# Optimization experiments

Hardware: AMD Instinct MI355X
Metric: run time of the kernel (lower is better)

The kernel has to match this reference:

```python
import jax, jax.numpy as jnp
import numpy as np

N_NODES = 100000


def gcn_conv(x, src, dst, W, b, n_nodes):
    # PyG GCNConv: h = X W; out[i] = sum_j norm_ij * h[j] + b, with self-loops
    # and symmetric normalization norm_ij = deg(i)^-1/2 * deg(j)^-1/2.
    h = x @ W  # [N, out]
    deg = jax.ops.segment_sum(jnp.ones_like(dst, dtype=h.dtype), dst, num_segments=n_nodes)
    dinv = jnp.where(deg > 0, jax.lax.rsqrt(deg), 0.0)
    norm = dinv[src] * dinv[dst]  # [E]
    msg = h[src] * norm[:, None]  # [E, out] gather + scale
    out = jax.ops.segment_sum(msg, dst, num_segments=n_nodes)  # scatter-add
    return out + b


def setup_inputs() -> dict:
    key = jax.random.key(0)
    k_x, k_e, k_w1, k_w2 = jax.random.split(key, 4)
    in_c, hid, out_c = 128, 64, 32
    x = jax.random.normal(k_x, (N_NODES, in_c), dtype=jnp.float32)
    edge_index = jax.random.randint(k_e, (2, 1600000), 0, N_NODES, dtype=jnp.int32)
    W1 = jax.random.normal(k_w1, (in_c, hid), dtype=jnp.float32) / np.sqrt(in_c)
    b1 = jnp.zeros((hid,), dtype=jnp.float32)
    W2 = jax.random.normal(k_w2, (hid, out_c), dtype=jnp.float32) / np.sqrt(hid)
    b2 = jnp.zeros((out_c,), dtype=jnp.float32)
    return {"x": x, "edge_index": edge_index, "W1": W1, "b1": b1, "W2": W2, "b2": b2}


def reference(x, edge_index, W1, b1, W2, b2):
    n = x.shape[0]
    # add self-loops (GCNConv default)
    loops = jnp.arange(n, dtype=edge_index.dtype)
    src = jnp.concatenate([edge_index[0], loops])
    dst = jnp.concatenate([edge_index[1], loops])
    # faithful to original forward: x = (x*x)/x
    x = (x * x) / x
    h = jax.nn.relu(gcn_conv(x, src, dst, W1, b1, n))
    return gcn_conv(h, src, dst, W2, b2, n)
```

## Files before the change

kernel.cpp:

```cpp
#include <hip/hip_runtime.h>
#include <hip/hip_fp16.h>


#define IN_C 128
#define HID 64
#define OUTC 32
#define BSH 9
#define BSZ 512
#define NSLOT 256
#define EPB 8192
#define BSTRIDE 9216

typedef _Float16 half8 __attribute__((ext_vector_type(8)));
typedef float f32x4 __attribute__((ext_vector_type(4)));

static __host__ __device__ __forceinline__ size_t szt(int a) { return (size_t)a; }

__global__ __launch_bounds__(256) void k_part(const int* __restrict__ src,
                                              const int* __restrict__ dst, int E,
                                              int* __restrict__ bedges,
                                              int* __restrict__ cnt,
                                              int* __restrict__ pre) {
  __shared__ int dbuf[EPB];
  __shared__ int sorted[EPB];
  __shared__ int h[NSLOT];
  __shared__ int off[NSLOT];
  const int tid = threadIdx.x;
  h[tid] = 0;
  __syncthreads();
  const int e0 = blockIdx.x * EPB;
  const int n = min(EPB, E - e0);
  const int nv = n & ~3;
  for (int i = tid * 4; i < nv; i += 1024) {
    int4 d4 = *reinterpret_cast<const int4*>(&dst[e0 + i]);
    dbuf[i + 0] = d4.x; dbuf[i + 1] = d4.y;
    dbuf[i + 2] = d4.z; dbuf[i + 3] = d4.w;
    atomicAdd(&h[d4.x >> BSH], 1);
    atomicAdd(&h[d4.y >> BSH], 1);
    atomicAdd(&h[d4.z >> BSH], 1);
    atomicAdd(&h[d4.w >> BSH], 1);
  }
  for (int i = nv + tid; i < n; i += 256) {
    int d = dst[e0 + i];
    dbuf[i] = d;
    atomicAdd(&h[d >> BSH], 1);
  }
  __syncthreads();
  int v = h[tid];
  off[tid] = v;
  __syncthreads();
  for (int o = 1; o < 256; o <<= 1) {
    int w = (tid >= o) ? off[tid - o] : 0;
    __syncthreads();
    off[tid] += w;
    __syncthreads();
  }
  int excl = off[tid] - v;
  cnt[blockIdx.x * NSLOT + tid] = v;
  pre[blockIdx.x * NSLOT + tid] = excl;
  __syncthreads();
  off[tid] = excl;
  __syncthreads();
  for (int i = tid * 4; i < nv; i += 1024) {
    int4 s4 = *reinterpret_cast<const int4*>(&src[e0 + i]);
    int d0 = dbuf[i], d1 = dbuf[i + 1], d2 = dbuf[i + 2], d3 = dbuf[i + 3];
    int p0 = atomicAdd(&off[d0 >> BSH], 1);
    sorted[p0] = (s4.x << BSH) | (d0 & (BSZ - 1));
    int p1 = atomicAdd(&off[d1 >> BSH], 1);
    sorted[p1] = (s4.y << BSH) | (d1 & (BSZ - 1));
    int p2 = atomicAdd(&off[d2 >> BSH], 1);
    sorted[p2] = (s4.z << BSH) | (d2 & (BSZ - 1));
    int p3 = atomicAdd(&off[d3 >> BSH], 1);
    sorted[p3] = (s4.w << BSH) | (d3 & (BSZ - 1));
  }
  for (int i = nv + tid; i < n; i += 256) {
    int s = src[e0 + i], d = dbuf[i];
    int p = atomicAdd(&off[d >> BSH], 1);
    sorted[p] = (s << BSH) | (d & (BSZ - 1));
  }
  __syncthreads();
  for (int i = tid * 4; i < nv; i += 1024) {
    *reinterpret_cast<int4*>(&bedges[e0 + i]) =
        make_int4(sorted[i], sorted[i + 1], sorted[i + 2], sorted[i + 3]);
  }
  for (int i = nv + tid; i < n; i += 256) bedges[e0 + i] = sorted[i];
}

__global__ __launch_bounds__(256) void k_bucket(const int* __restrict__ bedges,
                                                const int* __restrict__ cnt,
                                                const int* __restrict__ pre,
                                                int B, int E,
                                                int2* __restrict__ rd,
                                                float* __restrict__ dinv,
                                                int* __restrict__ csr, int N) {
  __shared__ int ebuf[BSTRIDE];
  __shared__ int obuf[BSTRIDE];
  __shared__ int h[BSZ];
  __shared__ int pfx[BSZ];
  __shared__ int c2[BSZ];
  __shared__ int sc[256];
  __shared__ int dsto[256];
  const int k = blockIdx.x;
  const int tid = threadIdx.x;
  h[tid] = 0; h[tid + 256] = 0;
  c2[tid] = 0; c2[tid + 256] = 0;
  int c = 0, so = 0;
  if (tid < B) {
    c = cnt[tid * NSLOT + k];
    so = pre[tid * NSLOT + k];
  }
  sc[tid] = c;
  __syncthreads();
  for (int o = 1; o < 256; o <<= 1) {
    int w = (tid >= o) ? sc[tid - o] : 0;
    __syncthreads();
    sc[tid] += w;
    __syncthreads();
  }
  dsto[tid] = sc[tid] - c;
  __syncthreads();
  int total = sc[255];
  int nE = min(total, BSTRIDE);
  if (tid < B && c > 0) {
    int gbase = tid * EPB + so;
    int dbase = dsto[tid];
    for (int j = 0; j < c; ++j) {
      int p = dbase + j;
      if (p < BSTRIDE) ebuf[p] = bedges[gbase + j];
    }
  }
  __syncthreads();
  for (int i = tid; i < nE; i += 256) atomicAdd(&h[ebuf[i] & (BSZ - 1)], 1);
  __syncthreads();
  int a0 = h[2 * tid], a1 = h[2 * tid + 1];
  int s = a0 + a1;
  sc[tid] = s;
  __syncthreads();
  for (int o = 1; o < 256; o <<= 1) {
    int w = (tid >= o) ? sc[tid - o] : 0;
    __syncthreads();
    sc[tid] += w;
    __syncthreads();
  }
  int ex = sc[tid] - s;
  pfx[2 * tid] = ex;
  pfx[2 * tid + 1] = ex + a0;
  __syncthreads();
  const int base = k * BSTRIDE;
  for (int i = tid; i < BSZ; i += 256) {
    int node = k * BSZ + i;
    if (node < N) {
      int dg = h[i];
      rd[node] = make_int2(base + pfx[i], dg);
      dinv[node] = rsqrtf((float)(dg + 1));
    }
  }
  for (int i = tid; i < nE; i += 256) {
    int e = ebuf[i];
    int l = e & (BSZ - 1);
    int p = pfx[l] + atomicAdd(&c2[l], 1);
    obuf[p] = e >> BSH;
  }
  __syncthreads();
  int nv = nE & ~3;
  for (int i = tid * 4; i < nv; i += 1024) {
    *reinterpret_cast<int4*>(&csr[base + i]) =
        make_int4(obuf[i], obuf[i + 1], obuf[i + 2], obuf[i + 3]);
  }
  for (int i = nv + tid; i < nE; i += 256) csr[base + i] = obuf[i];
}

__global__ __launch_bounds__(256) void k_gemm1(
    const float* __restrict__ x, const float* __restrict__ W1,
    const float* __restrict__ dinv, __half* __restrict__ h1s, int N) {
  __shared__ _Float16 bf[4 * 4 * 64 * 8];
  const int tid = threadIdx.x;
  for (int idx = tid; idx < 128 * 64; idx += 256) {
    int k = idx >> 6, c = idx & 63;
    int kc = k >> 5, kk = k & 31;
    int chunk = kk >> 3, j = kk & 7;
    int ct = c >> 4, cl = c & 15;
    bf[(((kc * 4 + ct) * 64) + chunk * 16 + cl) * 8 + j] = (_Float16)W1[idx];
  }
  __syncthreads();

  const int lane = tid & 63, wave = tid >> 6;
  const int row0 = blockIdx.x * 64 + wave * 16;
  const int r_a = lane & 15;
  const int chk = lane >> 4;
  const int arow = min(row0 + r_a, N - 1);
  const float* xp = x + szt(arow) * IN_C + chk * 8;

  f32x4 acc[4];
  #pragma unroll
  for (int ct = 0; ct < 4; ++ct) acc[ct] = (f32x4){0.f, 0.f, 0.f, 0.f};

  #pragma unroll
  for (int kc = 0; kc < 4; ++kc) {
    float4 a0 = *reinterpret_cast<const float4*>(xp + kc * 32);
    float4 a1v = *reinterpret_cast<const float4*>(xp + kc * 32 + 4);
    half8 af;
    af[0] = (_Float16)a0.x;  af[1] = (_Float16)a0.y;
    af[2] = (_Float16)a0.z;  af[3] = (_Float16)a0.w;
    af[4] = (_Float16)a1v.x; af[5] = (_Float16)a1v.y;
    af[6] = (_Float16)a1v.z; af[7] = (_Float16)a1v.w;
    #pragma unroll
    for (int ct = 0; ct < 4; ++ct) {
      half8 bfrag = *reinterpret_cast<const half8*>(&bf[(((kc * 4 + ct) * 64) + lane) * 8]);
      acc[ct] = __builtin_amdgcn_mfma_f32_16x16x32_f16(af, bfrag, acc[ct], 0, 0, 0);
    }
  }
  #pragma unroll
  for (int r = 0; r < 4; ++r) {
    int drow = row0 + chk * 4 + r;
    if (drow < N) {
      float di = dinv[drow];
      #pragma unroll
      for (int ct = 0; ct < 4; ++ct)
        h1s[szt(drow) * HID + ct * 16 + r_a] = (__half)(acc[ct][r] * di);
    }
  }
}

__global__ __launch_bounds__(256) void k_agg1(
    const __half* __restrict__ h1s, const int* __restrict__ csr,
    const int2* __restrict__ rd, const float* __restrict__ dinv,
    const float* __restrict__ b1, __half* __restrict__ a1, int N) {
  const int tid = threadIdx.x;
  int node = blockIdx.x * 32 + (tid >> 3);
  if (node >= N) return;
  const int l = tid & 7;
  const int g0 = (tid & 63) & ~7;
  const _Float16* hp = (const _Float16*)h1s;

  half8 selfv = *reinterpret_cast<const half8*>(hp + szt(node) * HID + l * 8);
  float acc[8];
  #pragma unroll
  for (int q = 0; q < 8; ++q) acc[q] = (float)selfv[q];

  int2 v = rd[node];
  int base = v.x, cnt = v.y;
  if (cnt > 0) {
    int last = base + cnt - 1;
    int myidx = csr[min(base + l, last)];
    for (int j = 0; j < cnt; j += 8) {
      int id[8];
      #pragma unroll
      for (int u = 0; u < 8; ++u) id[u] = __shfl(myidx, g0 + u);
      half8 gv[8];
      #pragma unroll
      for (int u = 0; u < 8; ++u)
        gv[u] = *reinterpret_cast<const half8*>(hp + szt(id[u]) * HID + l * 8);
      int jn = j + 8;
      if (jn < cnt) myidx = csr[min(base + jn + l, last)];
      #pragma unroll
      for (int u = 0; u < 8; ++u) {
        bool ok = (j + u) < cnt;
        #pragma unroll
        for (int q = 0; q < 8; ++q) acc[q] += ok ? (float)gv[u][q] : 0.0f;
      }
    }
  }
  float di = dinv[node];
  float4 bb0 = *reinterpret_cast<const float4*>(b1 + l * 8);
  float4 bb1 = *reinterpret_cast<const float4*>(b1 + l * 8 + 4);
  half8 o;
  o[0] = (_Float16)fmaxf(di * acc[0] + bb0.x, 0.f);
  o[1] = (_Float16)fmaxf(di * acc[1] + bb0.y, 0.f);
  o[2] = (_Float16)fmaxf(di * acc[2] + bb0.z, 0.f);
  o[3] = (_Float16)fmaxf(di * acc[3] + bb0.w, 0.f);
  o[4] = (_Float16)fmaxf(di * acc[4] + bb1.x, 0.f);
  o[5] = (_Float16)fmaxf(di * acc[5] + bb1.y, 0.f);
  o[6] = (_Float16)fmaxf(di * acc[6] + bb1.z, 0.f);
  o[7] = (_Float16)fmaxf(di * acc[7] + bb1.w, 0.f);
  *reinterpret_cast<half8*>((_Float16*)a1 + szt(node) * HID + l * 8) = o;
}

__global__ __launch_bounds__(256) void k_gemm2(
    const __half* __restrict__ a1, const float* __restrict__ W2,
    const float* __restrict__ dinv, __half* __restrict__ h2s, int N) {
  __shared__ _Float16 bf[2 * 2 * 64 * 8];
  const int tid = threadIdx.x;
  for (int idx = tid; idx < 64 * 32; idx += 256) {
    int k = idx >> 5, c = idx & 31;
    int kc = k >> 5, kk = k & 31;
    int chunk = kk >> 3, j = kk & 7;
    int ct = c >> 4, cl = c & 15;
    bf[(((kc * 2 + ct) * 64) + chunk * 16 + cl) * 8 + j] = (_Float16)W2[idx];
  }
  __syncthreads();

  const int lane = tid & 63, wave = tid >> 6;
  const int row0 = blockIdx.x * 64 + wave * 16;
  const int r_a = lane & 15;
  const int chk = lane >> 4;
  const int arow = min(row0 + r_a, N - 1);
  const _Float16* ap = (const _Float16*)a1 + szt(arow) * HID + chk * 8;

  f32x4 acc[2];
  acc[0] = (f32x4){0.f, 0.f, 0.f, 0.f};
  acc[1] = (f32x4){0.f, 0.f, 0.f, 0.f};
  #pragma unroll
  for (int kc = 0; kc < 2; ++kc) {
    half8 af = *reinterpret_cast<const half8*>(ap + kc * 32);
    #pragma unroll
    for (int ct = 0; ct < 2; ++ct) {
      half8 bfrag = *reinterpret_cast<const half8*>(&bf[(((kc * 2 + ct) * 64) + lane) * 8]);
      acc[ct] = __builtin_amdgcn_mfma_f32_16x16x32_f16(af, bfrag, acc[ct], 0, 0, 0);
    }
  }
  #pragma unroll
  for (int r = 0; r < 4; ++r) {
    int drow = row0 + chk * 4 + r;
    if (drow < N) {
      float di = dinv[drow];
      #pragma unroll
      for (int ct = 0; ct < 2; ++ct)
        h2s[szt(drow) * OUTC + ct * 16 + r_a] = (__half)(acc[ct][r] * di);
    }
  }
}

__global__ __launch_bounds__(256) void k_agg2(
    const __half* __restrict__ h2s, const int* __restrict__ csr,
    const int2* __restrict__ rd, const float* __restrict__ dinv,
    const float* __restrict__ b2, float* __restrict__ out, int N) {
  const int tid = threadIdx.x;
  int node = blockIdx.x * 64 + (tid >> 2);
  if (node >= N) return;
  const int l = tid & 3;
  const int g0 = (tid & 63) & ~3;
  const _Float16* hp = (const _Float16*)h2s;

  half8 selfv = *reinterpret_cast<const half8*>(hp + szt(node) * OUTC + l * 8);
  float acc[8];
  #pragma unroll
  for (int q = 0; q < 8; ++q) acc[q] = (float)selfv[q];

  int2 v = rd[node];
  int base = v.x, cnt = v.y;
  if (cnt > 0) {
    int last = base + cnt - 1;
    int myA = csr[min(base + 2 * l, last)];
    int myB = csr[min(base + 2 * l + 1, last)];
    for (int j = 0; j < cnt; j += 8) {
      int id[8];
      #pragma unroll
      for (int u = 0; u < 4; ++u) {
        id[2 * u]     = __shfl(myA, g0 + u);
        id[2 * u + 1] = __shfl(myB, g0 + u);
      }
      half8 gv[8];
      #pragma unroll
      for (int u = 0; u < 8; ++u)
        gv[u] = *reinterpret_cast<const half8*>(hp + szt(id[u]) * OUTC + l * 8);
      int jn = j + 8;
      if (jn < cnt) {
        myA = csr[min(base + jn + 2 * l, last)];
        myB = csr[min(base + jn + 2 * l + 1, last)];
      }
      #pragma unroll
      for (int u = 0; u < 8; ++u) {
        bool ok = (j + u) < cnt;
        #pragma unroll
        for (int q = 0; q < 8; ++q) acc[q] += ok ? (float)gv[u][q] : 0.0f;
      }
    }
  }
  float di = dinv[node];
  float4 bb0 = *reinterpret_cast<const float4*>(b2 + l * 8);
  float4 bb1 = *reinterpret_cast<const float4*>(b2 + l * 8 + 4);
  float4 o0, o1;
  o0.x = di * acc[0] + bb0.x; o0.y = di * acc[1] + bb0.y;
  o0.z = di * acc[2] + bb0.z; o0.w = di * acc[3] + bb0.w;
  o1.x = di * acc[4] + bb1.x; o1.y = di * acc[5] + bb1.y;
  o1.z = di * acc[6] + bb1.z; o1.w = di * acc[7] + bb1.w;
  float* op = out + szt(node) * OUTC + l * 8;
  *reinterpret_cast<float4*>(op) = o0;
  *reinterpret_cast<float4*>(op + 4) = o1;
}

extern "C" void kernel_launch(void* const* d_in, const int* in_sizes, int n_in,
                              void* d_out, int out_size, void* d_ws, size_t ws_size,
                              hipStream_t stream) {
  const float* x  = (const float*)d_in[0];
  const int*   ei = (const int*)d_in[1];
  const float* W1 = (const float*)d_in[2];
  const float* b1 = (const float*)d_in[3];
  const float* W2 = (const float*)d_in[4];
  const float* b2 = (const float*)d_in[5];
  float* out = (float*)d_out;

  const int N = in_sizes[0] / IN_C;
  const int E = in_sizes[1] / 2;
  const int* src = ei;
  const int* dst = ei + E;

  const int B   = (E + EPB - 1) / EPB;
  const int NBK = (N + BSZ - 1) / BSZ;

  char* ws = (char*)d_ws;
  size_t off = 0;
  auto alloc = [&](size_t bytes) {
    off = (off + 255) & ~(size_t)255;
    void* p = ws + off;
    off += bytes;
    return p;
  };
  int*    cnt    = (int*)alloc(szt(B) * NSLOT * 4);
  int*    pre    = (int*)alloc(szt(B) * NSLOT * 4);
  int2*   rd     = (int2*)alloc(szt(N) * 8);
  float*  dinv   = (float*)alloc(szt(N) * 4);
  int*    bedges = (int*)alloc(szt(B) * EPB * 4);
  int*    csr    = (int*)alloc(szt(NBK) * BSTRIDE * 4);
  __half* h1s    = (__half*)alloc(szt(N) * HID * 2);
  __half* a1     = (__half*)alloc(szt(N) * HID * 2);
  __half* h2s    = (__half*)alloc(szt(N) * OUTC * 2);
  (void)ws_size;

  k_part<<<B, 256, 0, stream>>>(src, dst, E, bedges, cnt, pre);
  k_bucket<<<NBK, 256, 0, stream>>>(bedges, cnt, pre, B, E, rd, dinv, csr, N);
  k_gemm1<<<(N + 63) / 64, 256, 0, stream>>>(x, W1, dinv, h1s, N);
  k_agg1<<<(N + 31) / 32, 256, 0, stream>>>(h1s, csr, rd, dinv, b1, a1, N);
  k_gemm2<<<(N + 63) / 64, 256, 0, stream>>>(a1, W2, dinv, h2s, N);
  k_agg2<<<(N + 63) / 64, 256, 0, stream>>>(h2s, csr, rd, dinv, b2, out, N);
}
```

Before: 118.7 us.

## Fuse layer-1 aggregation with layer-2 GEMM through shared memory

Merges the first aggregation kernel and the second GEMM into one kernel: each block aggregates 32 nodes, writes the ReLU'd activations into an LDS tile, then two waves run MFMA against W2 staged in LDS and write h2s directly. This removes the a1 global round-trip (write and reread of N×64 halves) and one kernel launch. In exchange every block re-stages W2 into LDS, adds a __syncthreads barrier after the irregular gather, and leaves half the waves idle during the MFMA phase.

```diff
diff --git a/kernel.cpp b/kernel.cpp
--- a/kernel.cpp
+++ b/kernel.cpp
@@ -222,65 +222,16 @@
   }
 }
 
-__global__ __launch_bounds__(256) void k_agg1(
+__global__ __launch_bounds__(256) void k_agg1f(
     const __half* __restrict__ h1s, const int* __restrict__ csr,
     const int2* __restrict__ rd, const float* __restrict__ dinv,
-    const float* __restrict__ b1, __half* __restrict__ a1, int N) {
+    const float* __restrict__ b1, const float* __restrict__ W2,
+    __half* __restrict__ h2s, int N) {
+  __shared__ _Float16 bf[2 * 2 * 64 * 8];
+  __shared__ _Float16 a1t[32 * 72];
+  __shared__ float dinv_s[32];
   const int tid = threadIdx.x;
-  int node = blockIdx.x * 32 + (tid >> 3);
-  if (node >= N) return;
-  const int l = tid & 7;
-  const int g0 = (tid & 63) & ~7;
-  const _Float16* hp = (const _Float16*)h1s;
-
-  half8 selfv = *reinterpret_cast<const half8*>(hp + szt(node) * HID + l * 8);
-  float acc[8];
-  #pragma unroll
-  for (int q = 0; q < 8; ++q) acc[q] = (float)selfv[q];
-
-  int2 v = rd[node];
-  int base = v.x, cnt = v.y;
-  if (cnt > 0) {
-    int last = base + cnt - 1;
-    int myidx = csr[min(base + l, last)];
-    for (int j = 0; j < cnt; j += 8) {
-      int id[8];
-      #pragma unroll
-      for (int u = 0; u < 8; ++u) id[u] = __shfl(myidx, g0 + u);
-      half8 gv[8];
-      #pragma unroll
-      for (int u = 0; u < 8; ++u)
-        gv[u] = *reinterpret_cast<const half8*>(hp + szt(id[u]) * HID + l * 8);
-      int jn = j + 8;
-      if (jn < cnt) myidx = csr[min(base + jn + l, last)];
-      #pragma unroll
-      for (int u = 0; u < 8; ++u) {
-        bool ok = (j + u) < cnt;
-        #pragma unroll
-        for (int q = 0; q < 8; ++q) acc[q] += ok ? (float)gv[u][q] : 0.0f;
-      }
-    }
-  }
-  float di = dinv[node];
-  float4 bb0 = *reinterpret_cast<const float4*>(b1 + l * 8);
-  float4 bb1 = *reinterpret_cast<const float4*>(b1 + l * 8 + 4);
-  half8 o;
-  o[0] = (_Float16)fmaxf(di * acc[0] + bb0.x, 0.f);
-  o[1] = (_Float16)fmaxf(di * acc[1] + bb0.y, 0.f);
-  o[2] = (_Float16)fmaxf(di * acc[2] + bb0.z, 0.f);
-  o[3] = (_Float16)fmaxf(di * acc[3] + bb0.w, 0.f);
-  o[4] = (_Float16)fmaxf(di * acc[4] + bb1.x, 0.f);
-  o[5] = (_Float16)fmaxf(di * acc[5] + bb1.y, 0.f);
-  o[6] = (_Float16)fmaxf(di * acc[6] + bb1.z, 0.f);
-  o[7] = (_Float16)fmaxf(di * acc[7] + bb1.w, 0.f);
-  *reinterpret_cast<half8*>((_Float16*)a1 + szt(node) * HID + l * 8) = o;
-}
-
-__global__ __launch_bounds__(256) void k_gemm2(
-    const __half* __restrict__ a1, const float* __restrict__ W2,
-    const float* __restrict__ dinv, __half* __restrict__ h2s, int N) {
-  __shared__ _Float16 bf[2 * 2 * 64 * 8];
-  const int tid = threadIdx.x;
+
   for (int idx = tid; idx < 64 * 32; idx += 256) {
     int k = idx >> 5, c = idx & 31;
     int kc = k >> 5, kk = k & 31;
@@ -288,35 +239,89 @@
     int ct = c >> 4, cl = c & 15;
     bf[(((kc * 2 + ct) * 64) + chunk * 16 + cl) * 8 + j] = (_Float16)W2[idx];
   }
-  __syncthreads();
-
-  const int lane = tid & 63, wave = tid >> 6;
-  const int row0 = blockIdx.x * 64 + wave * 16;
-  const int r_a = lane & 15;
-  const int chk = lane >> 4;
-  const int arow = min(row0 + r_a, N - 1);
-  const _Float16* ap = (const _Float16*)a1 + szt(arow) * HID + chk * 8;
-
-  f32x4 acc[2];
-  acc[0] = (f32x4){0.f, 0.f, 0.f, 0.f};
-  acc[1] = (f32x4){0.f, 0.f, 0.f, 0.f};
+
+  const int nl = tid >> 3;
+  const int node = blockIdx.x * 32 + nl;
+  const int l = tid & 7;
+  const int g0 = (tid & 63) & ~7;
+  const _Float16* hp = (const _Float16*)h1s;
+  half8 o;
   #pragma unroll
-  for (int kc = 0; kc < 2; ++kc) {
-    half8 af = *reinterpret_cast<const half8*>(ap + kc * 32);
+  for (int q = 0; q < 8; ++q) o[q] = (_Float16)0.f;
+  if (node < N) {
+    half8 selfv = *reinterpret_cast<const half8*>(hp + szt(node) * HID + l * 8);
+    float acc[8];
     #pragma unroll
-    for (int ct = 0; ct < 2; ++ct) {
-      half8 bfrag = *reinterpret_cast<const half8*>(&bf[(((kc * 2 + ct) * 64) + lane) * 8]);
-      acc[ct] = __builtin_amdgcn_mfma_f32_16x16x32_f16(af, bfrag, acc[ct], 0, 0, 0);
-    }
-  }
-  #pragma unroll
-  for (int r = 0; r < 4; ++r) {
-    int drow = row0 + chk * 4 + r;
-    if (drow < N) {
-      float di = dinv[drow];
+    for (int q = 0; q < 8; ++q) acc[q] = (float)selfv[q];
+    int2 v = rd[node];
+    int base = v.x, cnt = v.y;
+    if (cnt > 0) {
+      int last = base + cnt - 1;
+      int myidx = csr[min(base + l, last)];
+      for (int j = 0; j < cnt; j += 8) {
+        int id[8];
+        #pragma unroll
+        for (int u = 0; u < 8; ++u) id[u] = __shfl(myidx, g0 + u);
+        half8 gv[8];
+        #pragma unroll
+        for (int u = 0; u < 8; ++u)
+          gv[u] = *reinterpret_cast<const half8*>(hp + szt(id[u]) * HID + l * 8);
+        int jn = j + 8;
+        if (jn < cnt) myidx = csr[min(base + jn + l, last)];
+        #pragma unroll
+        for (int u = 0; u < 8; ++u) {
+          bool ok = (j + u) < cnt;
+          #pragma unroll
+          for (int q = 0; q < 8; ++q) acc[q] += ok ? (float)gv[u][q] : 0.0f;
+        }
+      }
+    }
+    float di = dinv[node];
+    float4 bb0 = *reinterpret_cast<const float4*>(b1 + l * 8);
+    float4 bb1 = *reinterpret_cast<const float4*>(b1 + l * 8 + 4);
+    o[0] = (_Float16)fmaxf(di * acc[0] + bb0.x, 0.f);
+    o[1] = (_Float16)fmaxf(di * acc[1] + bb0.y, 0.f);
+    o[2] = (_Float16)fmaxf(di * acc[2] + bb0.z, 0.f);
+    o[3] = (_Float16)fmaxf(di * acc[3] + bb0.w, 0.f);
+    o[4] = (_Float16)fmaxf(di * acc[4] + bb1.x, 0.f);
+    o[5] = (_Float16)fmaxf(di * acc[5] + bb1.y, 0.f);
+    o[6] = (_Float16)fmaxf(di * acc[6] + bb1.z, 0.f);
+    o[7] = (_Float16)fmaxf(di * acc[7] + bb1.w, 0.f);
+    if (l == 0) dinv_s[nl] = di;
+  } else {
+    if (l == 0) dinv_s[nl] = 0.f;
+  }
+  *reinterpret_cast<half8*>(&a1t[nl * 72 + l * 8]) = o;
+  __syncthreads();
+
+  const int wave = tid >> 6;
+  if (wave < 2) {
+    const int lane = tid & 63;
+    const int r_a = lane & 15;
+    const int chk = lane >> 4;
+    const int tr = wave * 16 + r_a;
+    f32x4 acc2[2];
+    acc2[0] = (f32x4){0.f, 0.f, 0.f, 0.f};
+    acc2[1] = (f32x4){0.f, 0.f, 0.f, 0.f};
+    #pragma unroll
+    for (int kc = 0; kc < 2; ++kc) {
+      half8 af = *reinterpret_cast<const half8*>(&a1t[tr * 72 + chk * 8 + kc * 32]);
       #pragma unroll
-      for (int ct = 0; ct < 2; ++ct)
-        h2s[szt(drow) * OUTC + ct * 16 + r_a] = (__half)(acc[ct][r] * di);
+      for (int ct = 0; ct < 2; ++ct) {
+        half8 bfrag = *reinterpret_cast<const half8*>(&bf[(((kc * 2 + ct) * 64) + lane) * 8]);
+        acc2[ct] = __builtin_amdgcn_mfma_f32_16x16x32_f16(af, bfrag, acc2[ct], 0, 0, 0);
+      }
+    }
+    #pragma unroll
+    for (int r = 0; r < 4; ++r) {
+      int drow = wave * 16 + chk * 4 + r;
+      int onode = blockIdx.x * 32 + drow;
+      if (onode < N) {
+        float di = dinv_s[drow];
+        #pragma unroll
+        for (int ct = 0; ct < 2; ++ct)
+          h2s[szt(onode) * OUTC + ct * 16 + r_a] = (__half)(acc2[ct][r] * di);
+      }
     }
   }
 }
@@ -414,14 +419,12 @@
   int*    bedges = (int*)alloc(szt(B) * EPB * 4);
   int*    csr    = (int*)alloc(szt(NBK) * BSTRIDE * 4);
   __half* h1s    = (__half*)alloc(szt(N) * HID * 2);
-  __half* a1     = (__half*)alloc(szt(N) * HID * 2);
   __half* h2s    = (__half*)alloc(szt(N) * OUTC * 2);
   (void)ws_size;
 
   k_part<<<B, 256, 0, stream>>>(src, dst, E, bedges, cnt, pre);
   k_bucket<<<NBK, 256, 0, stream>>>(bedges, cnt, pre, B, E, rd, dinv, csr, N);
   k_gemm1<<<(N + 63) / 64, 256, 0, stream>>>(x, W1, dinv, h1s, N);
-  k_agg1<<<(N + 31) / 32, 256, 0, stream>>>(h1s, csr, rd, dinv, b1, a1, N);
-  k_gemm2<<<(N + 63) / 64, 256, 0, stream>>>(a1, W2, dinv, h2s, N);
+  k_agg1f<<<(N + 31) / 32, 256, 0, stream>>>(h1s, csr, rd, dinv, b1, W2, h2s, N);
   k_agg2<<<(N + 63) / 64, 256, 0, stream>>>(h2s, csr, rd, dinv, b2, out, N);
 }
```

New measurement: 113.5 us. 1.05x faster.
